# Kernel tuning notes

Hardware: AMD Instinct MI355X
Metric: run time of the kernel (lower is better)

Reference implementation:

```python
import jax, jax.numpy as jnp
import numpy as np

N_NODES = 50000
N_EDGES = 800000
D = 64  # in_feat == hidden_channels


def _param(key, shape, fan_in):
    return jax.random.normal(key, shape, dtype=jnp.float32) / np.sqrt(fan_in)


def setup_inputs() -> dict:
    key = jax.random.key(0)
    ks = jax.random.split(key, 32)
    inp = {
        "x": jax.random.normal(ks[0], (N_NODES, D), dtype=jnp.float32),
        "edge_index": jax.random.randint(ks[1], (2, N_EDGES), 0, N_NODES, dtype=jnp.int64),
    }
    i = 2
    for l in (1, 2, 3):
        inp[f"W1_{l}"] = _param(ks[i + 0], (D, D), D)   # LEConv lin1 (source nodes)
        inp[f"b1_{l}"] = jnp.zeros((D,), jnp.float32)
        inp[f"W2_{l}"] = _param(ks[i + 1], (D, D), D)   # LEConv lin2 (target nodes, no bias)
        inp[f"W3_{l}"] = _param(ks[i + 2], (D, D), D)   # LEConv lin3 (root/self)
        inp[f"b3_{l}"] = jnp.zeros((D,), jnp.float32)
        inp[f"Wl_{l}"] = _param(ks[i + 3], (D, D), D)   # post-conv Linear
        inp[f"bl_{l}"] = jnp.zeros((D,), jnp.float32)
        i += 4
    return inp


def _leconv(x, src, dst, W1, b1, W2, W3, b3):
    # out_i = lin3(x_i) + sum_{j->i} (lin1(x_j) - lin2(x_i))
    a = x @ W1 + b1          # [N, D]
    b = x @ W2               # [N, D]
    msg = a[src] - b[dst]    # [E, D]  gather + elementwise
    agg = jax.ops.segment_sum(msg, dst, num_segments=x.shape[0])  # scatter-add
    return agg + (x @ W3 + b3)


def reference(x, edge_index,
              W1_1, b1_1, W2_1, W3_1, b3_1, Wl_1, bl_1,
              W1_2, b1_2, W2_2, W3_2, b3_2, Wl_2, bl_2,
              W1_3, b1_3, W2_3, W3_3, b3_3, Wl_3, bl_3):
    src, dst = edge_index[0], edge_index[1]
    h = x
    for (W1, b1, W2, W3, b3, Wl, bl) in (
        (W1_1, b1_1, W2_1, W3_1, b3_1, Wl_1, bl_1),
        (W1_2, b1_2, W2_2, W3_2, b3_2, Wl_2, bl_2),
        (W1_3, b1_3, W2_3, W3_3, b3_3, Wl_3, bl_3),
    ):
        h = _leconv(h, src, dst, W1, b1, W2, W3, b3)
        h = jax.nn.relu(h @ Wl + bl)
    return h
```

## Files before the change

kernel.cpp:

```cpp
#include <hip/hip_runtime.h>

#define N_NODES 50000
#define N_EDGES 800000
#define SCAN_NB ((N_NODES + 255) / 256)
#define NCHUNK 64
#define NRANGE 4
#define RNODES (N_NODES / NRANGE)
#define CEDGES (N_EDGES / NCHUNK)

typedef __attribute__((ext_vector_type(8))) short short8;
typedef __attribute__((ext_vector_type(4))) float f32x4;

struct LPtrs { const float *W1, *W2, *W3, *Wl, *b1, *b3, *bl; };
struct AllPtrs { LPtrs l[3]; };

__device__ inline unsigned short f2b(float f) {
    union { float f; unsigned u; } c; c.f = f;
    return (unsigned short)((c.u + 0x7FFFu + ((c.u >> 16) & 1u)) >> 16);
}
__device__ inline float b2f(unsigned short h) {
    union { unsigned u; float f; } c; c.u = ((unsigned)h) << 16;
    return c.f;
}

__global__ __launch_bounds__(256) void histp_kernel(const int* __restrict__ dst,
                                                    unsigned short* __restrict__ hist_part) {
    __shared__ int h[RNODES];
    const int chunk = blockIdx.x >> 2;
    const int range = blockIdx.x & 3;
    const int nbase = range * RNODES;
    for (int i = threadIdx.x; i < RNODES; i += 256) h[i] = 0;
    __syncthreads();
    const int* dp = dst + chunk * CEDGES;
    for (int i = threadIdx.x; i < CEDGES; i += 256) {
        int d = dp[i] - nbase;
        if ((unsigned)d < (unsigned)RNODES) atomicAdd(&h[d], 1);
    }
    __syncthreads();
    unsigned short* out = hist_part + (long)chunk * N_NODES + nbase;
    for (int i = threadIdx.x; i < RNODES; i += 256) out[i] = (unsigned short)h[i];
}

__global__ __launch_bounds__(256) void scanA2_kernel(unsigned short* __restrict__ hist_part,
                                                     int* __restrict__ off,
                                                     int* __restrict__ deg,
                                                     int* __restrict__ bsum) {
    __shared__ int tmp[256];
    const int t = threadIdx.x;
    const int node = blockIdx.x * 256 + t;
    int run = 0;
    if (node < N_NODES) {
        #pragma unroll
        for (int c = 0; c < NCHUNK; ++c) {
            unsigned short* p = hist_part + (long)c * N_NODES + node;
            int v = *p;
            *p = (unsigned short)run;
            run += v;
        }
        deg[node] = run;
    }
    int v = run;
    tmp[t] = v;
    __syncthreads();
    #pragma unroll
    for (int d = 1; d < 256; d <<= 1) {
        int u = (t >= d) ? tmp[t - d] : 0;
        __syncthreads();
        tmp[t] += u;
        __syncthreads();
    }
    if (node < N_NODES) off[node] = tmp[t] - v;
    if (t == 255) bsum[blockIdx.x] = tmp[255];
}

__global__ __launch_bounds__(256) void scanB_kernel(const int* __restrict__ bsum,
                                                    int* __restrict__ boff) {
    __shared__ int tmp[256];
    const int t = threadIdx.x;
    int v = (t < SCAN_NB) ? bsum[t] : 0;
    tmp[t] = v;
    __syncthreads();
    #pragma unroll
    for (int d = 1; d < 256; d <<= 1) {
        int u = (t >= d) ? tmp[t - d] : 0;
        __syncthreads();
        tmp[t] += u;
        __syncthreads();
    }
    if (t < SCAN_NB) boff[t] = tmp[t] - v;
}

__global__ __launch_bounds__(256) void fillp_kernel(const int* __restrict__ src,
                                                    const int* __restrict__ dst,
                                                    const int* __restrict__ off,
                                                    const int* __restrict__ boff,
                                                    const unsigned short* __restrict__ hist_part,
                                                    int* __restrict__ csr) {
    __shared__ int cur[RNODES];
    const int chunk = blockIdx.x >> 2;
    const int range = blockIdx.x & 3;
    const int nbase = range * RNODES;
    const unsigned short* bp = hist_part + (long)chunk * N_NODES + nbase;
    const int* op = off + nbase;
    for (int i = threadIdx.x; i < RNODES; i += 256)
        cur[i] = op[i] + boff[(nbase + i) >> 8] + (int)bp[i];
    __syncthreads();
    const int* dp = dst + chunk * CEDGES;
    const int* sp = src + chunk * CEDGES;
    for (int i = threadIdx.x; i < CEDGES; i += 256) {
        int d = dp[i] - nbase;
        if ((unsigned)d < (unsigned)RNODES) {
            int pos = atomicAdd(&cur[d], 1);
            csr[pos] = sp[i];
        }
    }
}

__global__ __launch_bounds__(256) void pack_mm_kernel(AllPtrs ap,
                                                      unsigned short* __restrict__ Wp,
                                                      float* __restrict__ rows)
{
    __shared__ float sW[64][65];
    __shared__ float sL[64][17];
    const int layer = blockIdx.x / 12;
    const int ct = blockIdx.x % 12;
    LPtrs L = ap.l[layer];
    const float* Wm = (ct < 4) ? L.W1 : (ct < 8) ? L.W2 : L.W3;
    const int colb = (ct & 3) * 16;

    for (int i = threadIdx.x; i < 64 * 64; i += 256) sW[i >> 6][i & 63] = Wm[i];
    for (int i = threadIdx.x; i < 64 * 16; i += 256) {
        int q = i >> 4, c = i & 15;
        sL[q][c] = L.Wl[q * 64 + colb + c];
    }
    __syncthreads();

    for (int local = threadIdx.x; local < 1024; local += 256) {
        int j = local & 7, lane = (local >> 3) & 63, s = local >> 9;
        int k = s * 32 + (lane >> 4) * 8 + j;
        int c = lane & 15;
        float acc = 0.f;
        #pragma unroll 8
        for (int q = 0; q < 64; ++q) acc += sW[k][q] * sL[q][c];
        Wp[layer * 12288 + ct * 1024 + local] = f2b(acc);
    }

    if (ct == 0 && threadIdx.x < 64) {
        int col = threadIdx.x;
        float r1 = 0.f, r3 = 0.f;
        for (int q = 0; q < 64; ++q) {
            float wl = L.Wl[q * 64 + col];
            r1 += L.b1[q] * wl;
            r3 += L.b3[q] * wl;
        }
        rows[layer * 128 + col] = r1;
        rows[layer * 128 + 64 + col] = r3 + L.bl[col];
    }
}

__global__ __launch_bounds__(256) void gemm3w_kernel(
    const unsigned short* __restrict__ hbf, const float* __restrict__ hf32,
    const unsigned short* __restrict__ Wp,
    const int* __restrict__ deg, const float* __restrict__ rows,
    unsigned short* __restrict__ abf, unsigned short* __restrict__ wbf, int n)
{
    const int t = threadIdx.x;
    const int lane = t & 63;
    const int quad = lane >> 4, lm = lane & 15;
    const int row_base = blockIdx.x * 64 + (t >> 6) * 16;

    int arow = min(row_base + lm, n - 1);
    short8 a0, a1;
    if (hf32) {
        const float* hrow = hf32 + (long)arow * 64;
        #pragma unroll
        for (int j = 0; j < 8; ++j) {
            a0[j] = (short)f2b(hrow[quad * 8 + j]);
            a1[j] = (short)f2b(hrow[32 + quad * 8 + j]);
        }
    } else {
        const unsigned short* hrow = hbf + (long)arow * 64;
        a0 = *(const short8*)(hrow + quad * 8);
        a1 = *(const short8*)(hrow + 32 + quad * 8);
    }

    const short8* wp = (const short8*)Wp;
    f32x4 acc[12];
    #pragma unroll
    for (int ct = 0; ct < 12; ++ct) {
        f32x4 z = {0.f, 0.f, 0.f, 0.f};
        short8 w0 = wp[(ct * 2 + 0) * 64 + lane];
        short8 w1 = wp[(ct * 2 + 1) * 64 + lane];
        z = __builtin_amdgcn_mfma_f32_16x16x32_bf16(a0, w0, z, 0, 0, 0);
        z = __builtin_amdgcn_mfma_f32_16x16x32_bf16(a1, w1, z, 0, 0, 0);
        acc[ct] = z;
    }

    const int g0 = row_base + quad * 4;
    float dg[4];
    #pragma unroll
    for (int r = 0; r < 4; ++r) dg[r] = (float)deg[min(g0 + r, n - 1)];

    #pragma unroll
    for (int ct = 0; ct < 4; ++ct) {
        int col = ct * 16 + lm;
        float r1 = rows[col];
        float r3 = rows[64 + col];
        #pragma unroll
        for (int r = 0; r < 4; ++r) {
            int g = g0 + r;
            if (g < n) {
                abf[(long)g * 64 + col] = f2b(acc[ct][r]);
                float wv = acc[8 + ct][r] - dg[r] * (acc[4 + ct][r] - r1) + r3;
                wbf[(long)g * 64 + col] = f2b(wv);
            }
        }
    }
}

__global__ __launch_bounds__(256) void gather_out_kernel(
    const int* __restrict__ off, const int* __restrict__ boff,
    const int* __restrict__ degv, const int* __restrict__ csr,
    const unsigned short* __restrict__ abf,
    const unsigned short* __restrict__ wbf,
    float* __restrict__ out_f, unsigned short* __restrict__ out_b, int last)
{
    int node = blockIdx.x * 4 + (threadIdx.x >> 6);
    int lane = threadIdx.x & 63;
    const int g = lane >> 3;
    const int f = (lane & 7) * 8;
    int beg = off[node] + boff[node >> 8];
    int end = beg + degv[node];
    float acc[8];
    #pragma unroll
    for (int q = 0; q < 8; ++q) acc[q] = 0.f;
    int j = beg;
    for (; j + 16 <= end; j += 16) {
        int s0 = csr[j + g], s1 = csr[j + 8 + g];
        short8 v0 = *(const short8*)(abf + (long)s0 * 64 + f);
        short8 v1 = *(const short8*)(abf + (long)s1 * 64 + f);
        #pragma unroll
        for (int q = 0; q < 8; ++q)
            acc[q] += b2f((unsigned short)v0[q]) + b2f((unsigned short)v1[q]);
    }
    for (; j < end; j += 8) {
        int jj = j + g;
        if (jj < end) {
            int s0 = csr[jj];
            short8 v0 = *(const short8*)(abf + (long)s0 * 64 + f);
            #pragma unroll
            for (int q = 0; q < 8; ++q) acc[q] += b2f((unsigned short)v0[q]);
        }
    }
    #pragma unroll
    for (int m = 8; m < 64; m <<= 1) {
        #pragma unroll
        for (int q = 0; q < 8; ++q) acc[q] += __shfl_xor(acc[q], m, 64);
    }
    if (g == 0) {
        short8 wv = *(const short8*)(wbf + (long)node * 64 + f);
        float o[8];
        #pragma unroll
        for (int q = 0; q < 8; ++q)
            o[q] = fmaxf(acc[q] + b2f((unsigned short)wv[q]), 0.f);
        if (last) {
            float4 o0 = {o[0], o[1], o[2], o[3]};
            float4 o1 = {o[4], o[5], o[6], o[7]};
            *(float4*)(out_f + (long)node * 64 + f) = o0;
            *(float4*)(out_f + (long)node * 64 + f + 4) = o1;
        } else {
            short8 ob;
            #pragma unroll
            for (int q = 0; q < 8; ++q) ob[q] = (short)f2b(o[q]);
            *(short8*)(out_b + (long)node * 64 + f) = ob;
        }
    }
}

extern "C" void kernel_launch(void* const* d_in, const int* in_sizes, int n_in,
                              void* d_out, int out_size, void* d_ws, size_t ws_size,
                              hipStream_t stream) {
    const float* x  = (const float*)d_in[0];
    const int*   ei = (const int*)d_in[1];
    const int*   src = ei;
    const int*   dst = ei + N_EDGES;

    char* wsb = (char*)d_ws;
    unsigned short* hist_part = (unsigned short*)(wsb);
    unsigned short* abf  = (unsigned short*)(wsb + 12800000);
    unsigned short* wbf  = (unsigned short*)(wsb + 19200000);
    unsigned short* h1   = (unsigned short*)(wsb + 25600000);
    unsigned short* Wp   = (unsigned short*)(wsb + 38400000);
    float*          rows = (float*)(wsb + 38500000);
    int* off  = (int*)(wsb + 38600000);
    int* deg  = off + N_NODES;
    int* bsum = deg + N_NODES;
    int* boff = bsum + SCAN_NB;
    int* csr  = boff + SCAN_NB;

    const int NBLK = (N_NODES + 63) / 64;

    histp_kernel<<<NCHUNK * NRANGE, 256, 0, stream>>>(dst, hist_part);
    scanA2_kernel<<<SCAN_NB, 256, 0, stream>>>(hist_part, off, deg, bsum);
    scanB_kernel<<<1, 256, 0, stream>>>(bsum, boff);
    fillp_kernel<<<NCHUNK * NRANGE, 256, 0, stream>>>(src, dst, off, boff, hist_part, csr);

    AllPtrs ap;
    for (int l = 0; l < 3; ++l) {
        int base = 2 + l * 7;
        ap.l[l].W1 = (const float*)d_in[base + 0];
        ap.l[l].b1 = (const float*)d_in[base + 1];
        ap.l[l].W2 = (const float*)d_in[base + 2];
        ap.l[l].W3 = (const float*)d_in[base + 3];
        ap.l[l].b3 = (const float*)d_in[base + 4];
        ap.l[l].Wl = (const float*)d_in[base + 5];
        ap.l[l].bl = (const float*)d_in[base + 6];
    }
    pack_mm_kernel<<<36, 256, 0, stream>>>(ap, Wp, rows);

    const unsigned short* hin = nullptr;
    for (int l = 0; l < 3; ++l) {
        const unsigned short* wp = Wp + l * 12288;
        gemm3w_kernel<<<NBLK, 256, 0, stream>>>(
            hin, (l == 0) ? x : nullptr, wp, deg, rows + l * 128,
            abf, wbf, N_NODES);

        int last = (l == 2);
        gather_out_kernel<<<N_NODES / 4, 256, 0, stream>>>(
            off, boff, deg, csr, abf, wbf, (float*)d_out, h1, last);
        hin = h1;
    }
}
```

Before: 276.8 us.

## Fuse CSR build and weight packing into one persistent kernel with grid barriers

Merges the histogram, two scan phases, CSR fill and weight-packing kernels into a single 256-block kernel separated by software grid barriers, with the weight packing running alongside the first scan. The goal is to remove four kernel launches and the gaps between them. It adds a memset for the barrier counters and depends on all 256 blocks being co-resident (each uses about 50KB of shared memory), which leaves a deadlock risk if they are not.

```diff
diff --git a/kernel.cpp b/kernel.cpp
--- a/kernel.cpp
+++ b/kernel.cpp
@@ -7,6 +7,7 @@
 #define NRANGE 4
 #define RNODES (N_NODES / NRANGE)
 #define CEDGES (N_EDGES / NCHUNK)
+#define GRID_CSR (NCHUNK * NRANGE)
 
 typedef __attribute__((ext_vector_type(8))) short short8;
 typedef __attribute__((ext_vector_type(4))) float f32x4;
@@ -23,138 +24,157 @@
     return c.f;
 }
 
-__global__ __launch_bounds__(256) void histp_kernel(const int* __restrict__ dst,
-                                                    unsigned short* __restrict__ hist_part) {
+__device__ inline void gridbar(int* bar) {
+    __syncthreads();
+    if (threadIdx.x == 0) {
+        __threadfence();
+        int gen = atomicAdd(&bar[1], 0);
+        int old = atomicAdd(&bar[0], 1);
+        if (old == GRID_CSR - 1) {
+            bar[0] = 0;
+            __threadfence();
+            atomicAdd(&bar[1], 1);
+        } else {
+            while (atomicAdd(&bar[1], 0) == gen) {}
+        }
+        __threadfence();
+    }
+    __syncthreads();
+}
+
+__global__ __launch_bounds__(256) void csr_pack_kernel(
+    const int* __restrict__ src, const int* __restrict__ dst,
+    AllPtrs ap,
+    unsigned short* __restrict__ hist_part,
+    int* __restrict__ off, int* __restrict__ deg,
+    int* __restrict__ bsum, int* __restrict__ boff,
+    int* __restrict__ csr,
+    unsigned short* __restrict__ Wp, float* __restrict__ rows,
+    int* __restrict__ bar)
+{
     __shared__ int h[RNODES];
-    const int chunk = blockIdx.x >> 2;
-    const int range = blockIdx.x & 3;
-    const int nbase = range * RNODES;
-    for (int i = threadIdx.x; i < RNODES; i += 256) h[i] = 0;
-    __syncthreads();
-    const int* dp = dst + chunk * CEDGES;
-    for (int i = threadIdx.x; i < CEDGES; i += 256) {
-        int d = dp[i] - nbase;
-        if ((unsigned)d < (unsigned)RNODES) atomicAdd(&h[d], 1);
-    }
-    __syncthreads();
-    unsigned short* out = hist_part + (long)chunk * N_NODES + nbase;
-    for (int i = threadIdx.x; i < RNODES; i += 256) out[i] = (unsigned short)h[i];
-}
-
-__global__ __launch_bounds__(256) void scanA2_kernel(unsigned short* __restrict__ hist_part,
-                                                     int* __restrict__ off,
-                                                     int* __restrict__ deg,
-                                                     int* __restrict__ bsum) {
-    __shared__ int tmp[256];
+    const int b = blockIdx.x;
     const int t = threadIdx.x;
-    const int node = blockIdx.x * 256 + t;
-    int run = 0;
-    if (node < N_NODES) {
-        #pragma unroll
-        for (int c = 0; c < NCHUNK; ++c) {
-            unsigned short* p = hist_part + (long)c * N_NODES + node;
-            int v = *p;
-            *p = (unsigned short)run;
-            run += v;
-        }
-        deg[node] = run;
-    }
-    int v = run;
-    tmp[t] = v;
-    __syncthreads();
-    #pragma unroll
-    for (int d = 1; d < 256; d <<= 1) {
-        int u = (t >= d) ? tmp[t - d] : 0;
-        __syncthreads();
-        tmp[t] += u;
-        __syncthreads();
-    }
-    if (node < N_NODES) off[node] = tmp[t] - v;
-    if (t == 255) bsum[blockIdx.x] = tmp[255];
-}
-
-__global__ __launch_bounds__(256) void scanB_kernel(const int* __restrict__ bsum,
-                                                    int* __restrict__ boff) {
-    __shared__ int tmp[256];
-    const int t = threadIdx.x;
-    int v = (t < SCAN_NB) ? bsum[t] : 0;
-    tmp[t] = v;
-    __syncthreads();
-    #pragma unroll
-    for (int d = 1; d < 256; d <<= 1) {
-        int u = (t >= d) ? tmp[t - d] : 0;
-        __syncthreads();
-        tmp[t] += u;
-        __syncthreads();
-    }
-    if (t < SCAN_NB) boff[t] = tmp[t] - v;
-}
-
-__global__ __launch_bounds__(256) void fillp_kernel(const int* __restrict__ src,
-                                                    const int* __restrict__ dst,
-                                                    const int* __restrict__ off,
-                                                    const int* __restrict__ boff,
-                                                    const unsigned short* __restrict__ hist_part,
-                                                    int* __restrict__ csr) {
-    __shared__ int cur[RNODES];
-    const int chunk = blockIdx.x >> 2;
-    const int range = blockIdx.x & 3;
-    const int nbase = range * RNODES;
-    const unsigned short* bp = hist_part + (long)chunk * N_NODES + nbase;
-    const int* op = off + nbase;
-    for (int i = threadIdx.x; i < RNODES; i += 256)
-        cur[i] = op[i] + boff[(nbase + i) >> 8] + (int)bp[i];
-    __syncthreads();
-    const int* dp = dst + chunk * CEDGES;
-    const int* sp = src + chunk * CEDGES;
-    for (int i = threadIdx.x; i < CEDGES; i += 256) {
-        int d = dp[i] - nbase;
-        if ((unsigned)d < (unsigned)RNODES) {
-            int pos = atomicAdd(&cur[d], 1);
-            csr[pos] = sp[i];
-        }
-    }
-}
-
-__global__ __launch_bounds__(256) void pack_mm_kernel(AllPtrs ap,
-                                                      unsigned short* __restrict__ Wp,
-                                                      float* __restrict__ rows)
-{
-    __shared__ float sW[64][65];
-    __shared__ float sL[64][17];
-    const int layer = blockIdx.x / 12;
-    const int ct = blockIdx.x % 12;
-    LPtrs L = ap.l[layer];
-    const float* Wm = (ct < 4) ? L.W1 : (ct < 8) ? L.W2 : L.W3;
-    const int colb = (ct & 3) * 16;
-
-    for (int i = threadIdx.x; i < 64 * 64; i += 256) sW[i >> 6][i & 63] = Wm[i];
-    for (int i = threadIdx.x; i < 64 * 16; i += 256) {
-        int q = i >> 4, c = i & 15;
-        sL[q][c] = L.Wl[q * 64 + colb + c];
-    }
-    __syncthreads();
-
-    for (int local = threadIdx.x; local < 1024; local += 256) {
-        int j = local & 7, lane = (local >> 3) & 63, s = local >> 9;
-        int k = s * 32 + (lane >> 4) * 8 + j;
-        int c = lane & 15;
-        float acc = 0.f;
-        #pragma unroll 8
-        for (int q = 0; q < 64; ++q) acc += sW[k][q] * sL[q][c];
-        Wp[layer * 12288 + ct * 1024 + local] = f2b(acc);
-    }
-
-    if (ct == 0 && threadIdx.x < 64) {
-        int col = threadIdx.x;
-        float r1 = 0.f, r3 = 0.f;
-        for (int q = 0; q < 64; ++q) {
-            float wl = L.Wl[q * 64 + col];
-            r1 += L.b1[q] * wl;
-            r3 += L.b3[q] * wl;
-        }
-        rows[layer * 128 + col] = r1;
-        rows[layer * 128 + 64 + col] = r3 + L.bl[col];
+
+    {
+        const int chunk = b >> 2;
+        const int range = b & 3;
+        const int nbase = range * RNODES;
+        for (int i = t; i < RNODES; i += 256) h[i] = 0;
+        __syncthreads();
+        const int* dp = dst + chunk * CEDGES;
+        for (int i = t; i < CEDGES; i += 256) {
+            int d = dp[i] - nbase;
+            if ((unsigned)d < (unsigned)RNODES) atomicAdd(&h[d], 1);
+        }
+        __syncthreads();
+        unsigned short* out = hist_part + (long)chunk * N_NODES + nbase;
+        for (int i = t; i < RNODES; i += 256) out[i] = (unsigned short)h[i];
+    }
+    gridbar(bar);
+
+    if (b < SCAN_NB) {
+        int* tmp = h;
+        const int node = b * 256 + t;
+        int run = 0;
+        if (node < N_NODES) {
+            #pragma unroll
+            for (int c = 0; c < NCHUNK; ++c) {
+                unsigned short* p = hist_part + (long)c * N_NODES + node;
+                int v = *p;
+                *p = (unsigned short)run;
+                run += v;
+            }
+            deg[node] = run;
+        }
+        int v = run;
+        __syncthreads();
+        tmp[t] = v;
+        __syncthreads();
+        #pragma unroll
+        for (int d = 1; d < 256; d <<= 1) {
+            int u = (t >= d) ? tmp[t - d] : 0;
+            __syncthreads();
+            tmp[t] += u;
+            __syncthreads();
+        }
+        if (node < N_NODES) off[node] = tmp[t] - v;
+        if (t == 255) bsum[b] = tmp[255];
+    } else if (b < SCAN_NB + 36) {
+        float* sW = (float*)h;
+        float* sL = (float*)h + 64 * 65;
+        const int wi = b - SCAN_NB;
+        const int layer = wi / 12;
+        const int ct = wi % 12;
+        LPtrs L = ap.l[layer];
+        const float* Wm = (ct < 4) ? L.W1 : (ct < 8) ? L.W2 : L.W3;
+        const int colb = (ct & 3) * 16;
+        __syncthreads();
+        for (int i = t; i < 64 * 64; i += 256) sW[(i >> 6) * 65 + (i & 63)] = Wm[i];
+        for (int i = t; i < 64 * 16; i += 256) {
+            int q = i >> 4, c = i & 15;
+            sL[q * 17 + c] = L.Wl[q * 64 + colb + c];
+        }
+        __syncthreads();
+        for (int local = t; local < 1024; local += 256) {
+            int j = local & 7, lane = (local >> 3) & 63, s = local >> 9;
+            int k = s * 32 + (lane >> 4) * 8 + j;
+            int c = lane & 15;
+            float acc = 0.f;
+            #pragma unroll 8
+            for (int q = 0; q < 64; ++q) acc += sW[k * 65 + q] * sL[q * 17 + c];
+            Wp[layer * 12288 + ct * 1024 + local] = f2b(acc);
+        }
+        if (ct == 0 && t < 64) {
+            int col = t;
+            float r1 = 0.f, r3 = 0.f;
+            for (int q = 0; q < 64; ++q) {
+                float wl = L.Wl[q * 64 + col];
+                r1 += L.b1[q] * wl;
+                r3 += L.b3[q] * wl;
+            }
+            rows[layer * 128 + col] = r1;
+            rows[layer * 128 + 64 + col] = r3 + L.bl[col];
+        }
+    }
+    gridbar(bar);
+
+    if (b == 0) {
+        int* tmp = h;
+        int v = (t < SCAN_NB) ? bsum[t] : 0;
+        __syncthreads();
+        tmp[t] = v;
+        __syncthreads();
+        #pragma unroll
+        for (int d = 1; d < 256; d <<= 1) {
+            int u = (t >= d) ? tmp[t - d] : 0;
+            __syncthreads();
+            tmp[t] += u;
+            __syncthreads();
+        }
+        if (t < SCAN_NB) boff[t] = tmp[t] - v;
+    }
+    gridbar(bar);
+
+    {
+        const int chunk = b >> 2;
+        const int range = b & 3;
+        const int nbase = range * RNODES;
+        const unsigned short* bp = hist_part + (long)chunk * N_NODES + nbase;
+        const int* op = off + nbase;
+        int* cur = h;
+        for (int i = t; i < RNODES; i += 256)
+            cur[i] = op[i] + boff[(nbase + i) >> 8] + (int)bp[i];
+        __syncthreads();
+        const int* dp = dst + chunk * CEDGES;
+        const int* sp = src + chunk * CEDGES;
+        for (int i = t; i < CEDGES; i += 256) {
+            int d = dp[i] - nbase;
+            if ((unsigned)d < (unsigned)RNODES) {
+                int pos = atomicAdd(&cur[d], 1);
+                csr[pos] = sp[i];
+            }
+        }
     }
 }
 
@@ -296,14 +316,10 @@
     int* deg  = off + N_NODES;
     int* bsum = deg + N_NODES;
     int* boff = bsum + SCAN_NB;
-    int* csr  = boff + SCAN_NB;
+    int* bar  = boff + SCAN_NB;
+    int* csr  = bar + 2;
 
     const int NBLK = (N_NODES + 63) / 64;
-
-    histp_kernel<<<NCHUNK * NRANGE, 256, 0, stream>>>(dst, hist_part);
-    scanA2_kernel<<<SCAN_NB, 256, 0, stream>>>(hist_part, off, deg, bsum);
-    scanB_kernel<<<1, 256, 0, stream>>>(bsum, boff);
-    fillp_kernel<<<NCHUNK * NRANGE, 256, 0, stream>>>(src, dst, off, boff, hist_part, csr);
 
     AllPtrs ap;
     for (int l = 0; l < 3; ++l) {
@@ -316,7 +332,10 @@
         ap.l[l].Wl = (const float*)d_in[base + 5];
         ap.l[l].bl = (const float*)d_in[base + 6];
     }
-    pack_mm_kernel<<<36, 256, 0, stream>>>(ap, Wp, rows);
+
+    hipMemsetAsync(bar, 0, 2 * sizeof(int), stream);
+    csr_pack_kernel<<<GRID_CSR, 256, 0, stream>>>(
+        src, dst, ap, hist_part, off, deg, bsum, boff, csr, Wp, rows, bar);
 
     const unsigned short* hin = nullptr;
     for (int l = 0; l < 3; ++l) {
```

New measurement: 338.2 us. +22.2%, slower.
